# Performance work log

Hardware: AMD Instinct MI355X
Metric: run time of the kernel (lower is better)

## Reference

```python
import jax, jax.numpy as jnp
import numpy as np

N = 50000      # nodes
E = 800000     # edges
DIN = 256
DH = 256
DOUT = 64


def setup_inputs() -> dict:
    key = jax.random.key(0)
    ks = jax.random.split(key, 8)
    x = jax.random.normal(ks[0], (N, DIN), dtype=jnp.float32)
    edge_index = jax.random.randint(ks[1], (2, E), 0, N, dtype=jnp.int64)
    s = 0.05
    W1 = jax.random.normal(ks[2], (DIN, DH), dtype=jnp.float32) * s
    b1 = jnp.zeros((DH,), dtype=jnp.float32)
    W2 = jax.random.normal(ks[3], (DH, DH), dtype=jnp.float32) * s
    b2 = jnp.zeros((DH,), dtype=jnp.float32)
    W3 = jax.random.normal(ks[4], (DH, DOUT), dtype=jnp.float32) * s
    b3 = jnp.zeros((DOUT,), dtype=jnp.float32)
    return {"x": x, "edge_index": edge_index, "W1": W1, "b1": b1,
            "W2": W2, "b2": b2, "W3": W3, "b3": b3}


def gcn_conv(x, src, dst, deg_inv_sqrt, W, b):
    # x: [N, din] -> [N, dout]. PyG GCNConv: h = D^{-1/2}(A+I)D^{-1/2} (x W) + b
    n = x.shape[0]
    h = x @ W                                   # [N, dout]
    norm = deg_inv_sqrt[src] * deg_inv_sqrt[dst]  # [E+N]
    msgs = h[src] * norm[:, None]               # gather + scale, [E+N, dout]
    out = jax.ops.segment_sum(msgs, dst, num_segments=n)  # scatter-add
    return out + b


def _loops(edge_index, n):
    # add self loops, compute symmetric normalization degrees
    sl = jnp.arange(n, dtype=edge_index.dtype)
    src = jnp.concatenate([edge_index[0], sl])
    dst = jnp.concatenate([edge_index[1], sl])
    deg = jax.ops.segment_sum(jnp.ones_like(dst, dtype=jnp.float32), dst, num_segments=n)
    dis = jnp.where(deg > 0, jax.lax.rsqrt(deg), 0.0)
    return src, dst, dis


def reference(x, edge_index, W1, b1, W2, b2, W3, b3):
    src, dst, dis = _loops(edge_index, x.shape[0])
    h = jax.nn.relu(gcn_conv(x, src, dst, dis, W1, b1))   # dropout: eval no-op
    h = jax.nn.relu(gcn_conv(h, src, dst, dis, W2, b2))
    out = gcn_conv(h, src, dst, dis, W3, b3)              # batch=None -> no pooling
    return out
```

## Files before the change

kernel.cpp:

```cpp
#include <hip/hip_runtime.h>
#include <hip/hip_fp8.h>
#include <cstdint>
#include <cstddef>

typedef unsigned short u16;
typedef _Float16 f16x8 __attribute__((ext_vector_type(8)));
typedef float f32x2 __attribute__((ext_vector_type(2)));
typedef float f32x4 __attribute__((ext_vector_type(4)));

#if defined(__has_builtin)
#if __has_builtin(__builtin_amdgcn_cvt_pk_f32_fp8) && __has_builtin(__builtin_amdgcn_cvt_pk_fp8_f32)
#define FP8_BUILTIN 1
#endif
#endif

__device__ __forceinline__ float h2f(u16 u) {
  return (float)__builtin_bit_cast(_Float16, u);
}
__device__ __forceinline__ u16 f2h(float f) {
  return __builtin_bit_cast(u16, (_Float16)f);
}
__device__ __forceinline__ unsigned char ftofp8(float f) {
#ifdef FP8_BUILTIN
  return (unsigned char)(__builtin_amdgcn_cvt_pk_fp8_f32(f, f, 0, false) & 0xFF);
#else
  return __hip_fp8_e4m3(f).__x;
#endif
}

__device__ __forceinline__ void async16(u16* lds, const u16* g) {
  __builtin_amdgcn_global_load_lds(
      (const __attribute__((address_space(1))) unsigned int*)g,
      (__attribute__((address_space(3))) unsigned int*)lds, 16, 0, 0);
}

__device__ __forceinline__ void fma8p(float* a, float d, uint2 p) {
#ifdef FP8_BUILTIN
  f32x2 v0 = __builtin_amdgcn_cvt_pk_f32_fp8((int)p.x, false);
  f32x2 v1 = __builtin_amdgcn_cvt_pk_f32_fp8((int)p.x, true);
  f32x2 v2 = __builtin_amdgcn_cvt_pk_f32_fp8((int)p.y, false);
  f32x2 v3 = __builtin_amdgcn_cvt_pk_f32_fp8((int)p.y, true);
  a[0] += d * v0.x; a[1] += d * v0.y; a[2] += d * v1.x; a[3] += d * v1.y;
  a[4] += d * v2.x; a[5] += d * v2.y; a[6] += d * v3.x; a[7] += d * v3.y;
#else
  const unsigned char* b = (const unsigned char*)&p;
#pragma unroll
  for (int k = 0; k < 8; ++k) {
    __hip_fp8_e4m3 v; v.__x = b[k];
    a[k] += d * (float)v;
  }
#endif
}

__device__ __forceinline__ f16x8 cvt8(const float* p) {
  float4 a = *(const float4*)p;
  float4 b = *(const float4*)(p + 4);
  f16x8 r;
  r[0] = (_Float16)a.x; r[1] = (_Float16)a.y; r[2] = (_Float16)a.z; r[3] = (_Float16)a.w;
  r[4] = (_Float16)b.x; r[5] = (_Float16)b.y; r[6] = (_Float16)b.z; r[7] = (_Float16)b.w;
  return r;
}

__device__ __forceinline__ int wave_is64(const void* ep) {
  const unsigned* p = (const unsigned*)ep;
  const int lane = threadIdx.x & 63;
  unsigned v = p[2 * lane + 1] | p[2 * (lane + 64) + 1];
  unsigned long long bal = __ballot(v != 0u);
  return (bal == 0ull) ? 1 : 0;
}

__device__ __forceinline__ int edge_at(const void* ep, int is64, long long idx) {
  if (is64) return (int)((const long long*)ep)[idx];
  return ((const int*)ep)[idx];
}

#define NCHUNK 64

__global__ void zero_f32(float* p, int n) {
  int i = blockIdx.x * 256 + threadIdx.x;
  if (i < n) p[i] = 0.f;
}

__global__ __launch_bounds__(256) void prep_all(
    const float* __restrict__ W1, u16* __restrict__ wt1,
    const float* __restrict__ W2, u16* __restrict__ wt2,
    const float* __restrict__ W3, u16* __restrict__ wt3,
    const void* __restrict__ ep, int* __restrict__ cnt,
    int E, int N, int DIN, int DH, int DOUT,
    int nb_w1, int nb_w2, int nb_w3) {
  int b = blockIdx.x;
  if (b < nb_w1) {
    int idx = b * 256 + threadIdx.x;
    if (idx < DIN * DH) {
      int n = idx / DIN, k = idx % DIN;
      wt1[idx] = f2h(W1[k * DH + n]);
    }
    return;
  }
  b -= nb_w1;
  if (b < nb_w2) {
    int idx = b * 256 + threadIdx.x;
    if (idx < DH * DH) {
      int n = idx / DH, k = idx % DH;
      wt2[idx] = f2h(W2[k * DH + n]);
    }
    return;
  }
  b -= nb_w2;
  if (b < nb_w3) {
    int idx = b * 256 + threadIdx.x;
    if (idx < DH * DOUT) {
      int n = idx / DH, k = idx % DH;
      wt3[idx] = f2h(W3[k * DOUT + n]);
    }
    return;
  }
  b -= nb_w3;
  {
    __shared__ int h[256];
    h[threadIdx.x] = 0;
    __syncthreads();
    int is64 = wave_is64(ep);
    const int per = (E + NCHUNK - 1) / NCHUNK;
    const int e0 = b * per, e1 = min(e0 + per, E);
    for (int e = e0 + (int)threadIdx.x; e < e1; e += 256) {
      int d = edge_at(ep, is64, (long long)E + e);
      d = min(max(d, 0), N - 1);
      atomicAdd(&h[d >> 8], 1);
    }
    __syncthreads();
    cnt[threadIdx.x * NCHUNK + b] = h[threadIdx.x];
  }
}

__device__ __forceinline__ void bases_in_lds(const int* __restrict__ cnt,
                                             int nbuck, int E, int* bl, int* ws4) {
  const int t = threadIdx.x, lane = t & 63, w = t >> 6;
  int tot = 0;
  if (t < nbuck)
#pragma unroll 8
    for (int c = 0; c < NCHUNK; ++c) tot += cnt[t * NCHUNK + c];
  int inc = tot;
#pragma unroll
  for (int o = 1; o < 64; o <<= 1) {
    int u = __shfl_up(inc, o, 64);
    if (lane >= o) inc += u;
  }
  if (lane == 63) ws4[w] = inc;
  __syncthreads();
  if (t == 0) {
    int run = 0;
#pragma unroll
    for (int k = 0; k < 4; ++k) { int v = ws4[k]; ws4[k + 4] = run; run += v; }
  }
  __syncthreads();
  bl[t] = ws4[w + 4] + inc - tot;
  if (t == 0) bl[nbuck] = E;
  __syncthreads();
}

__global__ __launch_bounds__(256) void csr_bucket(const void* __restrict__ ep,
                                                  const int* __restrict__ cnt,
                                                  unsigned* __restrict__ tmp,
                                                  int E, int N, int nbuck) {
  __shared__ int bl[257];
  __shared__ int cur[256];
  __shared__ int ws4[8];
  const int chunk = blockIdx.x;
  const int t = threadIdx.x;
  bases_in_lds(cnt, nbuck, E, bl, ws4);
  if (t < nbuck) {
    int partial = 0;
    for (int c = 0; c < chunk; ++c) partial += cnt[t * NCHUNK + c];
    cur[t] = bl[t] + partial;
  }
  __syncthreads();
  int is64 = wave_is64(ep);
  const int per = (E + NCHUNK - 1) / NCHUNK;
  const int e0 = chunk * per, e1 = min(e0 + per, E);
  for (int e = e0 + t; e < e1; e += 256) {
    int s = edge_at(ep, is64, e);
    int d = edge_at(ep, is64, (long long)E + e);
    s = min(max(s, 0), N - 1);
    d = min(max(d, 0), N - 1);
    int pos = atomicAdd(&cur[d >> 8], 1);
    tmp[pos] = ((unsigned)d << 16) | (unsigned)s;
  }
}

__global__ __launch_bounds__(256) void csr_final(const unsigned* __restrict__ tmp,
                                                 const int* __restrict__ cnt,
                                                 int* __restrict__ rp,
                                                 float* __restrict__ dis,
                                                 u16* __restrict__ col,
                                                 int N, int E, int nbuck) {
  __shared__ int bl[257];
  __shared__ int hcnt[256];
  __shared__ int curs[256];
  __shared__ int ws4[8];
  const int b = blockIdx.x;
  const int node0 = b * 256;
  const int t = threadIdx.x, lane = t & 63, w = t >> 6;
  bases_in_lds(cnt, nbuck, E, bl, ws4);
  const int k0 = bl[b], k1 = bl[b + 1];
  hcnt[t] = 0;
  __syncthreads();
  for (int k = k0 + t; k < k1; k += 256)
    atomicAdd(&hcnt[(int)(tmp[k] >> 16) - node0], 1);
  __syncthreads();
  const int v = hcnt[t];
  int inc = v;
#pragma unroll
  for (int o = 1; o < 64; o <<= 1) {
    int u = __shfl_up(inc, o, 64);
    if (lane >= o) inc += u;
  }
  __syncthreads();
  if (lane == 63) ws4[w] = inc;
  __syncthreads();
  if (t == 0) {
    int run = 0;
#pragma unroll
    for (int k = 0; k < 4; ++k) { int vv = ws4[k]; ws4[k + 4] = run; run += vv; }
  }
  __syncthreads();
  const int excl = k0 + ws4[w + 4] + inc - v;
  if (node0 + t < N) {
    rp[node0 + t] = excl;
    dis[node0 + t] = rsqrtf((float)(v + 1));
  }
  if (b == 0 && t == 0) rp[N] = E;
  curs[t] = excl;
  __syncthreads();
  for (int k = k0 + t; k < k1; k += 256) {
    unsigned e = tmp[k];
    int dl = (int)(e >> 16) - node0;
    int pos = atomicAdd(&curs[dl], 1);
    col[pos] = (u16)(e & 0xFFFFu);
  }
}

template <int BN, int OUT8, int A32>
__global__ __launch_bounds__(256) void gemm_bres(const void* __restrict__ A,
                                                 const u16* __restrict__ Bt,
                                                 void* __restrict__ Cv, int Nt,
                                                 int Nrows) {
  constexpr int K = 256;
  constexpr int NJ = BN / 16;
  constexpr int CH = BN * K / 8;
  __shared__ __align__(16) u16 Bs[BN * K];

  const int tid = threadIdx.x, lane = tid & 63, w = tid >> 6;
  const int bm = blockIdx.x, bn = blockIdx.y;

#pragma unroll
  for (int i = 0; i < CH / 256; ++i) {
    int c = tid + i * 256;
    int ln = c & 63, t2 = c >> 6;
    int ks = t2 & 7, j = t2 >> 3;
    int row = j * 16 + (ln & 15);
    int kk = ks * 32 + (ln >> 4) * 8;
    async16(&Bs[(size_t)c * 8], Bt + (size_t)(bn * BN + row) * K + kk);
  }

  const int r16 = lane & 15, quad = lane >> 4;
  const int m0 = w * 32;

  int row0 = bm * 128 + m0 + r16;
  int row1 = row0 + 16;
  f16x8 aa0[8], aa1[8];
  if (A32) {
    row0 = min(row0, Nrows - 1);
    row1 = min(row1, Nrows - 1);
    const float* A0 = (const float*)A + (size_t)row0 * K + quad * 8;
    const float* A1 = (const float*)A + (size_t)row1 * K + quad * 8;
#pragma unroll
    for (int ks = 0; ks < 8; ++ks) {
      aa0[ks] = cvt8(A0 + ks * 32);
      aa1[ks] = cvt8(A1 + ks * 32);
    }
  } else {
    const u16* A0 = (const u16*)A + (size_t)row0 * K + quad * 8;
    const u16* A1 = (const u16*)A + (size_t)row1 * K + quad * 8;
#pragma unroll
    for (int ks = 0; ks < 8; ++ks) {
      aa0[ks] = *(const f16x8*)(A0 + ks * 32);
      aa1[ks] = *(const f16x8*)(A1 + ks * 32);
    }
  }

  f32x4 acc[2][NJ];
  const f32x4 fzero = {0.f, 0.f, 0.f, 0.f};
#pragma unroll
  for (int i = 0; i < 2; ++i)
#pragma unroll
    for (int j = 0; j < NJ; ++j) acc[i][j] = fzero;

  __syncthreads();

#pragma unroll
  for (int ks = 0; ks < 8; ++ks) {
#pragma unroll
    for (int j = 0; j < NJ; ++j) {
      f16x8 bf = *(const f16x8*)(&Bs[(size_t)((j * 8 + ks) * 64 + lane) * 8]);
      acc[0][j] = __builtin_amdgcn_mfma_f32_16x16x32_f16(aa0[ks], bf, acc[0][j], 0, 0, 0);
      acc[1][j] = __builtin_amdgcn_mfma_f32_16x16x32_f16(aa1[ks], bf, acc[1][j], 0, 0, 0);
    }
  }
#pragma unroll
  for (int i = 0; i < 2; ++i)
#pragma unroll
    for (int j = 0; j < NJ; ++j) {
      int gr = bm * 128 + m0 + i * 16 + quad * 4;
      int gc = bn * BN + j * 16 + r16;
#pragma unroll
      for (int r = 0; r < 4; ++r) {
        if (OUT8) {
          ((unsigned char*)Cv)[(size_t)(gr + r) * Nt + gc] = ftofp8(acc[i][j][r]);
        } else {
          ((u16*)Cv)[(size_t)(gr + r) * Nt + gc] = f2h(acc[i][j][r]);
        }
      }
    }
}

__global__ __launch_bounds__(256) void agg_d256(const unsigned char* __restrict__ h,
                                                const int* __restrict__ rp,
                                                const u16* __restrict__ col,
                                                const float* __restrict__ dis,
                                                const float* __restrict__ bias,
                                                u16* __restrict__ out, int N) {
  const int wid = threadIdx.x >> 6, lane = threadIdx.x & 63;
  const int i = blockIdx.x * 4 + wid;
  if (i >= N) return;
  const int sub = lane >> 5;
  const int l32 = lane & 31;
  const int c8 = l32 * 8;
  const float di = dis[i];
  float a[8] = {0.f, 0.f, 0.f, 0.f, 0.f, 0.f, 0.f, 0.f};
  if (sub == 0) {
    uint2 sv = *(const uint2*)(h + (size_t)i * 256 + c8);
    fma8p(a, di, sv);
  }
  const int e1 = rp[i + 1];
  for (int base = rp[i]; base < e1; base += 64) {
    int me = base + lane;
    int s_l = 0; float d_l = 0.f;
    if (me < e1) { s_l = (int)col[me]; d_l = dis[s_l]; }
    const int cnt = min(64, e1 - base);
    const int cntR = (cnt + 7) & ~7;
    for (int t = 0; t < cntR; t += 8) {
      int sA = __shfl(s_l, t + sub, 64);      float dA = __shfl(d_l, t + sub, 64);
      int sB = __shfl(s_l, t + 2 + sub, 64);  float dB = __shfl(d_l, t + 2 + sub, 64);
      int sC = __shfl(s_l, t + 4 + sub, 64);  float dC = __shfl(d_l, t + 4 + sub, 64);
      int sD = __shfl(s_l, t + 6 + sub, 64);  float dD = __shfl(d_l, t + 6 + sub, 64);
      uint2 pA = *(const uint2*)(h + (size_t)sA * 256 + c8);
      uint2 pB = *(const uint2*)(h + (size_t)sB * 256 + c8);
      uint2 pC = *(const uint2*)(h + (size_t)sC * 256 + c8);
      uint2 pD = *(const uint2*)(h + (size_t)sD * 256 + c8);
      fma8p(a, dA, pA); fma8p(a, dB, pB); fma8p(a, dC, pC); fma8p(a, dD, pD);
    }
  }
#pragma unroll
  for (int k = 0; k < 8; ++k) a[k] += __shfl_xor(a[k], 32, 64);
  if (sub == 0) {
    float4 b0 = *(const float4*)(bias + c8);
    float4 b1 = *(const float4*)(bias + c8 + 4);
    float r0 = fmaxf(di * a[0] + b0.x, 0.f), r1 = fmaxf(di * a[1] + b0.y, 0.f);
    float r2 = fmaxf(di * a[2] + b0.z, 0.f), r3 = fmaxf(di * a[3] + b0.w, 0.f);
    float r4 = fmaxf(di * a[4] + b1.x, 0.f), r5 = fmaxf(di * a[5] + b1.y, 0.f);
    float r6 = fmaxf(di * a[6] + b1.z, 0.f), r7 = fmaxf(di * a[7] + b1.w, 0.f);
    uint4 ov;
    ov.x = (unsigned)f2h(r0) | ((unsigned)f2h(r1) << 16);
    ov.y = (unsigned)f2h(r2) | ((unsigned)f2h(r3) << 16);
    ov.z = (unsigned)f2h(r4) | ((unsigned)f2h(r5) << 16);
    ov.w = (unsigned)f2h(r6) | ((unsigned)f2h(r7) << 16);
    *(uint4*)(out + (size_t)i * 256 + c8) = ov;
  }
}

__global__ __launch_bounds__(256) void agg_d64(const unsigned char* __restrict__ h,
                                               const int* __restrict__ rp,
                                               const u16* __restrict__ col,
                                               const float* __restrict__ dis,
                                               const float* __restrict__ bias,
                                               float* __restrict__ out, int N) {
  const int wid = threadIdx.x >> 6, lane = threadIdx.x & 63;
  const int i = blockIdx.x * 4 + wid;
  if (i >= N) return;
  const int grp = lane >> 3;
  const int l8 = lane & 7;
  const int c8 = l8 * 8;
  const float di = dis[i];
  float a[8] = {0.f, 0.f, 0.f, 0.f, 0.f, 0.f, 0.f, 0.f};
  if (grp == 0) {
    uint2 sv = *(const uint2*)(h + (size_t)i * 64 + c8);
    fma8p(a, di, sv);
  }
  const int e1 = rp[i + 1];
  for (int base = rp[i]; base < e1; base += 64) {
    int me = base + lane;
    int s_l = 0; float d_l = 0.f;
    if (me < e1) { s_l = (int)col[me]; d_l = dis[s_l]; }
    const int cnt = min(64, e1 - base);
    const int cntR = (cnt + 15) & ~15;
    for (int t = 0; t < cntR; t += 16) {
      int sA = __shfl(s_l, t + grp, 64);       float dA = __shfl(d_l, t + grp, 64);
      int sB = __shfl(s_l, t + 8 + grp, 64);   float dB = __shfl(d_l, t + 8 + grp, 64);
      uint2 pA = *(const uint2*)(h + (size_t)sA * 64 + c8);
      uint2 pB = *(const uint2*)(h + (size_t)sB * 64 + c8);
      fma8p(a, dA, pA); fma8p(a, dB, pB);
    }
  }
#pragma unroll
  for (int k = 0; k < 8; ++k) a[k] += __shfl_xor(a[k], 8, 64);
#pragma unroll
  for (int k = 0; k < 8; ++k) a[k] += __shfl_xor(a[k], 16, 64);
#pragma unroll
  for (int k = 0; k < 8; ++k) a[k] += __shfl_xor(a[k], 32, 64);
  if (lane < 8) {
    float4 b0 = *(const float4*)(bias + c8);
    float4 b1 = *(const float4*)(bias + c8 + 4);
    float4 o0, o1;
    o0.x = di * a[0] + b0.x; o0.y = di * a[1] + b0.y;
    o0.z = di * a[2] + b0.z; o0.w = di * a[3] + b0.w;
    o1.x = di * a[4] + b1.x; o1.y = di * a[5] + b1.y;
    o1.z = di * a[6] + b1.z; o1.w = di * a[7] + b1.w;
    *(float4*)(out + (size_t)i * 64 + c8) = o0;
    *(float4*)(out + (size_t)i * 64 + c8 + 4) = o1;
  }
}

extern "C" void kernel_launch(void* const* d_in, const int* in_sizes, int n_in,
                              void* d_out, int out_size, void* d_ws, size_t ws_size,
                              hipStream_t stream) {
  if (n_in < 8) return;
  const float* x = (const float*)d_in[0];
  const void* eptr = d_in[1];
  const float* W1 = (const float*)d_in[2];
  const float* b1 = (const float*)d_in[3];
  const float* W2 = (const float*)d_in[4];
  const float* b2 = (const float*)d_in[5];
  const float* W3 = (const float*)d_in[6];
  const float* b3 = (const float*)d_in[7];
  float* out = (float*)d_out;

  const int DIN = 256, DH = 256;
  const int N = in_sizes[0] / DIN;
  const int E = in_sizes[1] / 2;
  const int DOUT = in_sizes[6] / DH;
  const int MT = (N + 127) / 128;
  const int Mpad = MT * 128;
  const int nbuck = (N + 255) >> 8;

  auto rnd = [](size_t b) { return (b + 255) & ~(size_t)255; };
  size_t required = 0;
  required += rnd((size_t)Mpad * DH * 2);
  required += rnd((size_t)Mpad * DH);
  required += rnd((size_t)E * 2);
  required += rnd((size_t)E * 4);
  required += rnd((size_t)(N + 1) * 4);
  required += rnd((size_t)N * 4);
  required += rnd((size_t)DIN * DH * 2);
  required += rnd((size_t)DH * DH * 2);
  required += rnd((size_t)DH * DOUT * 2);
  required += rnd((size_t)256 * NCHUNK * 4);
  if (ws_size < required || N > 65536 || nbuck > 256 || nbuck < 1) {
    zero_f32<<<(out_size + 255) / 256, 256, 0, stream>>>(out, out_size);
    return;
  }

  char* ws = (char*)d_ws;
  size_t off0 = 0;
  auto alloc = [&](size_t bytes) {
    char* p = ws + off0;
    off0 = (off0 + bytes + 255) & ~(size_t)255;
    return p;
  };
  u16* xpad = (u16*)alloc((size_t)Mpad * DH * 2);
  unsigned char* hbuf = (unsigned char*)alloc((size_t)Mpad * DH);
  u16* colb = (u16*)alloc((size_t)E * 2);
  unsigned* tmpb = (unsigned*)alloc((size_t)E * 4);
  int* rp = (int*)alloc((size_t)(N + 1) * 4);
  float* dis = (float*)alloc((size_t)N * 4);
  u16* wt1 = (u16*)alloc((size_t)DIN * DH * 2);
  u16* wt2 = (u16*)alloc((size_t)DH * DH * 2);
  u16* wt3 = (u16*)alloc((size_t)DH * DOUT * 2);
  int* cnt = (int*)alloc((size_t)256 * NCHUNK * 4);

  const int nb_w1 = (DIN * DH + 255) / 256;
  const int nb_w2 = (DH * DH + 255) / 256;
  const int nb_w3 = (DH * DOUT + 255) / 256;
  prep_all<<<nb_w1 + nb_w2 + nb_w3 + NCHUNK, 256, 0, stream>>>(
      W1, wt1, W2, wt2, W3, wt3, eptr, cnt,
      E, N, DIN, DH, DOUT, nb_w1, nb_w2, nb_w3);

  csr_bucket<<<NCHUNK, 256, 0, stream>>>(eptr, cnt, tmpb, E, N, nbuck);
  csr_final<<<nbuck, 256, 0, stream>>>(tmpb, cnt, rp, dis, colb, N, E, nbuck);

  gemm_bres<128, 1, 1><<<dim3(MT, DH / 128), 256, 0, stream>>>(x, wt1, hbuf, DH, N);
  agg_d256<<<(N + 3) / 4, 256, 0, stream>>>(hbuf, rp, colb, dis, b1, xpad, N);
  gemm_bres<128, 1, 0><<<dim3(MT, DH / 128), 256, 0, stream>>>(xpad, wt2, hbuf, DH, N);
  agg_d256<<<(N + 3) / 4, 256, 0, stream>>>(hbuf, rp, colb, dis, b2, xpad, N);
  gemm_bres<64, 1, 0><<<dim3(MT, DOUT / 64), 256, 0, stream>>>(xpad, wt3, hbuf, DOUT, N);
  agg_d64<<<(N + 3) / 4, 256, 0, stream>>>(hbuf, rp, colb, dis, b3, out, N);
}
```

Baseline: 297.1 us.

## Fold source-degree scaling into aggregation outputs and use fp16 final layer

The aggregation kernels now multiply their output rows by the source normalization dis[i] before writing. The following GEMM therefore produces pre-scaled features, and the next aggregation no longer has to load and shuffle per-edge dis values. The second layer carries a ×4 fp8 scale that is undone at the end. The last GEMM writes fp16 instead of fp8, which doubles the gather bytes for the 64-wide layer. CSR chunking also grows from 64 to 256 with a transposed count layout for coalesced reads, and a guard is added for small E or DOUT != 64.

```diff
diff --git a/kernel.cpp b/kernel.cpp
--- a/kernel.cpp
+++ b/kernel.cpp
@@ -19,6 +19,9 @@
 }
 __device__ __forceinline__ u16 f2h(float f) {
   return __builtin_bit_cast(u16, (_Float16)f);
+}
+__device__ __forceinline__ unsigned pkh(float lo, float hi) {
+  return (unsigned)f2h(lo) | ((unsigned)f2h(hi) << 16);
 }
 __device__ __forceinline__ unsigned char ftofp8(float f) {
 #ifdef FP8_BUILTIN
@@ -34,22 +37,28 @@
       (__attribute__((address_space(3))) unsigned int*)lds, 16, 0, 0);
 }
 
-__device__ __forceinline__ void fma8p(float* a, float d, uint2 p) {
+__device__ __forceinline__ void fma8p2(f32x2* a2, float d, uint2 p) {
 #ifdef FP8_BUILTIN
+  f32x2 d2; d2[0] = d; d2[1] = d;
   f32x2 v0 = __builtin_amdgcn_cvt_pk_f32_fp8((int)p.x, false);
   f32x2 v1 = __builtin_amdgcn_cvt_pk_f32_fp8((int)p.x, true);
   f32x2 v2 = __builtin_amdgcn_cvt_pk_f32_fp8((int)p.y, false);
   f32x2 v3 = __builtin_amdgcn_cvt_pk_f32_fp8((int)p.y, true);
-  a[0] += d * v0.x; a[1] += d * v0.y; a[2] += d * v1.x; a[3] += d * v1.y;
-  a[4] += d * v2.x; a[5] += d * v2.y; a[6] += d * v3.x; a[7] += d * v3.y;
+  a2[0] += d2 * v0; a2[1] += d2 * v1; a2[2] += d2 * v2; a2[3] += d2 * v3;
 #else
   const unsigned char* b = (const unsigned char*)&p;
 #pragma unroll
   for (int k = 0; k < 8; ++k) {
     __hip_fp8_e4m3 v; v.__x = b[k];
-    a[k] += d * (float)v;
+    a2[k >> 1][k & 1] += d * (float)v;
   }
 #endif
+}
+
+__device__ __forceinline__ void fma8h(float* a, float d, uint4 p) {
+  const u16* q = (const u16*)&p;
+#pragma unroll
+  for (int k = 0; k < 8; ++k) a[k] += d * h2f(q[k]);
 }
 
 __device__ __forceinline__ f16x8 cvt8(const float* p) {
@@ -74,7 +83,7 @@
   return ((const int*)ep)[idx];
 }
 
-#define NCHUNK 64
+#define NCHUNK 256
 
 __global__ void zero_f32(float* p, int n) {
   int i = blockIdx.x * 256 + threadIdx.x;
@@ -129,7 +138,7 @@
       atomicAdd(&h[d >> 8], 1);
     }
     __syncthreads();
-    cnt[threadIdx.x * NCHUNK + b] = h[threadIdx.x];
+    cnt[b * 256 + threadIdx.x] = h[threadIdx.x];
   }
 }
 
@@ -137,9 +146,10 @@
                                              int nbuck, int E, int* bl, int* ws4) {
   const int t = threadIdx.x, lane = t & 63, w = t >> 6;
   int tot = 0;
-  if (t < nbuck)
-#pragma unroll 8
-    for (int c = 0; c < NCHUNK; ++c) tot += cnt[t * NCHUNK + c];
+  if (t < nbuck) {
+#pragma unroll 4
+    for (int c = 0; c < NCHUNK; ++c) tot += cnt[c * 256 + t];
+  }
   int inc = tot;
 #pragma unroll
   for (int o = 1; o < 64; o <<= 1) {
@@ -171,7 +181,7 @@
   bases_in_lds(cnt, nbuck, E, bl, ws4);
   if (t < nbuck) {
     int partial = 0;
-    for (int c = 0; c < chunk; ++c) partial += cnt[t * NCHUNK + c];
+    for (int c = 0; c < chunk; ++c) partial += cnt[c * 256 + t];
     cur[t] = bl[t] + partial;
   }
   __syncthreads();
@@ -240,7 +250,7 @@
   }
 }
 
-template <int BN, int OUT8, int A32>
+template <int BN, int OUT8, int A32, int SC>
 __global__ __launch_bounds__(256) void gemm_bres(const void* __restrict__ A,
                                                  const u16* __restrict__ Bt,
                                                  void* __restrict__ Cv, int Nt,
@@ -316,7 +326,8 @@
 #pragma unroll
       for (int r = 0; r < 4; ++r) {
         if (OUT8) {
-          ((unsigned char*)Cv)[(size_t)(gr + r) * Nt + gc] = ftofp8(acc[i][j][r]);
+          ((unsigned char*)Cv)[(size_t)(gr + r) * Nt + gc] =
+              ftofp8(acc[i][j][r] * (float)SC);
         } else {
           ((u16*)Cv)[(size_t)(gr + r) * Nt + gc] = f2h(acc[i][j][r]);
         }
@@ -324,6 +335,7 @@
     }
 }
 
+template <int SCALED>
 __global__ __launch_bounds__(256) void agg_d256(const unsigned char* __restrict__ h,
                                                 const int* __restrict__ rp,
                                                 const u16* __restrict__ col,
@@ -337,49 +349,67 @@
   const int l32 = lane & 31;
   const int c8 = l32 * 8;
   const float di = dis[i];
-  float a[8] = {0.f, 0.f, 0.f, 0.f, 0.f, 0.f, 0.f, 0.f};
+  f32x2 a2[4];
+#pragma unroll
+  for (int k = 0; k < 4; ++k) { a2[k][0] = 0.f; a2[k][1] = 0.f; }
   if (sub == 0) {
     uint2 sv = *(const uint2*)(h + (size_t)i * 256 + c8);
-    fma8p(a, di, sv);
+    fma8p2(a2, SCALED ? 1.f : di, sv);
   }
   const int e1 = rp[i + 1];
   for (int base = rp[i]; base < e1; base += 64) {
     int me = base + lane;
     int s_l = 0; float d_l = 0.f;
-    if (me < e1) { s_l = (int)col[me]; d_l = dis[s_l]; }
+    if (me < e1) { s_l = (int)col[me]; if (!SCALED) d_l = dis[s_l]; }
     const int cnt = min(64, e1 - base);
     const int cntR = (cnt + 7) & ~7;
     for (int t = 0; t < cntR; t += 8) {
-      int sA = __shfl(s_l, t + sub, 64);      float dA = __shfl(d_l, t + sub, 64);
-      int sB = __shfl(s_l, t + 2 + sub, 64);  float dB = __shfl(d_l, t + 2 + sub, 64);
-      int sC = __shfl(s_l, t + 4 + sub, 64);  float dC = __shfl(d_l, t + 4 + sub, 64);
-      int sD = __shfl(s_l, t + 6 + sub, 64);  float dD = __shfl(d_l, t + 6 + sub, 64);
+      int sA = __shfl(s_l, t + sub, 64);
+      int sB = __shfl(s_l, t + 2 + sub, 64);
+      int sC = __shfl(s_l, t + 4 + sub, 64);
+      int sD = __shfl(s_l, t + 6 + sub, 64);
+      float dA, dB, dC, dD;
+      if (SCALED) {
+        dA = (t + sub < cnt) ? 1.f : 0.f;
+        dB = (t + 2 + sub < cnt) ? 1.f : 0.f;
+        dC = (t + 4 + sub < cnt) ? 1.f : 0.f;
+        dD = (t + 6 + sub < cnt) ? 1.f : 0.f;
+      } else {
+        dA = __shfl(d_l, t + sub, 64);
+        dB = __shfl(d_l, t + 2 + sub, 64);
+        dC = __shfl(d_l, t + 4 + sub, 64);
+        dD = __shfl(d_l, t + 6 + sub, 64);
+      }
       uint2 pA = *(const uint2*)(h + (size_t)sA * 256 + c8);
       uint2 pB = *(const uint2*)(h + (size_t)sB * 256 + c8);
       uint2 pC = *(const uint2*)(h + (size_t)sC * 256 + c8);
       uint2 pD = *(const uint2*)(h + (size_t)sD * 256 + c8);
-      fma8p(a, dA, pA); fma8p(a, dB, pB); fma8p(a, dC, pC); fma8p(a, dD, pD);
-    }
-  }
-#pragma unroll
-  for (int k = 0; k < 8; ++k) a[k] += __shfl_xor(a[k], 32, 64);
+      fma8p2(a2, dA, pA); fma8p2(a2, dB, pB);
+      fma8p2(a2, dC, pC); fma8p2(a2, dD, pD);
+    }
+  }
+#pragma unroll
+  for (int k = 0; k < 4; ++k) {
+    a2[k][0] += __shfl_xor(a2[k][0], 32, 64);
+    a2[k][1] += __shfl_xor(a2[k][1], 32, 64);
+  }
   if (sub == 0) {
+    const float inv = SCALED ? 0.25f : 1.f;
     float4 b0 = *(const float4*)(bias + c8);
     float4 b1 = *(const float4*)(bias + c8 + 4);
-    float r0 = fmaxf(di * a[0] + b0.x, 0.f), r1 = fmaxf(di * a[1] + b0.y, 0.f);
-    float r2 = fmaxf(di * a[2] + b0.z, 0.f), r3 = fmaxf(di * a[3] + b0.w, 0.f);
-    float r4 = fmaxf(di * a[4] + b1.x, 0.f), r5 = fmaxf(di * a[5] + b1.y, 0.f);
-    float r6 = fmaxf(di * a[6] + b1.z, 0.f), r7 = fmaxf(di * a[7] + b1.w, 0.f);
+    float bb[8] = {b0.x, b0.y, b0.z, b0.w, b1.x, b1.y, b1.z, b1.w};
+    float r[8];
+#pragma unroll
+    for (int k = 0; k < 8; ++k)
+      r[k] = fmaxf(di * a2[k >> 1][k & 1] * inv + bb[k], 0.f) * di;
     uint4 ov;
-    ov.x = (unsigned)f2h(r0) | ((unsigned)f2h(r1) << 16);
-    ov.y = (unsigned)f2h(r2) | ((unsigned)f2h(r3) << 16);
-    ov.z = (unsigned)f2h(r4) | ((unsigned)f2h(r5) << 16);
-    ov.w = (unsigned)f2h(r6) | ((unsigned)f2h(r7) << 16);
+    ov.x = pkh(r[0], r[1]); ov.y = pkh(r[2], r[3]);
+    ov.z = pkh(r[4], r[5]); ov.w = pkh(r[6], r[7]);
     *(uint4*)(out + (size_t)i * 256 + c8) = ov;
   }
 }
 
-__global__ __launch_bounds__(256) void agg_d64(const unsigned char* __restrict__ h,
+__global__ __launch_bounds__(256) void agg_d64(const u16* __restrict__ h,
                                                const int* __restrict__ rp,
                                                const u16* __restrict__ col,
                                                const float* __restrict__ dis,
@@ -394,22 +424,24 @@
   const float di = dis[i];
   float a[8] = {0.f, 0.f, 0.f, 0.f, 0.f, 0.f, 0.f, 0.f};
   if (grp == 0) {
-    uint2 sv = *(const uint2*)(h + (size_t)i * 64 + c8);
-    fma8p(a, di, sv);
+    uint4 sv = *(const uint4*)(h + (size_t)i * 64 + c8);
+    fma8h(a, 1.f, sv);
   }
   const int e1 = rp[i + 1];
   for (int base = rp[i]; base < e1; base += 64) {
     int me = base + lane;
-    int s_l = 0; float d_l = 0.f;
-    if (me < e1) { s_l = (int)col[me]; d_l = dis[s_l]; }
+    int s_l = 0;
+    if (me < e1) s_l = (int)col[me];
     const int cnt = min(64, e1 - base);
     const int cntR = (cnt + 15) & ~15;
     for (int t = 0; t < cntR; t += 16) {
-      int sA = __shfl(s_l, t + grp, 64);       float dA = __shfl(d_l, t + grp, 64);
-      int sB = __shfl(s_l, t + 8 + grp, 64);   float dB = __shfl(d_l, t + 8 + grp, 64);
-      uint2 pA = *(const uint2*)(h + (size_t)sA * 64 + c8);
-      uint2 pB = *(const uint2*)(h + (size_t)sB * 64 + c8);
-      fma8p(a, dA, pA); fma8p(a, dB, pB);
+      int sA = __shfl(s_l, t + grp, 64);
+      int sB = __shfl(s_l, t + 8 + grp, 64);
+      float dA = (t + grp < cnt) ? 1.f : 0.f;
+      float dB = (t + 8 + grp < cnt) ? 1.f : 0.f;
+      uint4 pA = *(const uint4*)(h + (size_t)sA * 64 + c8);
+      uint4 pB = *(const uint4*)(h + (size_t)sB * 64 + c8);
+      fma8h(a, dA, pA); fma8h(a, dB, pB);
     }
   }
 #pragma unroll
@@ -465,7 +497,8 @@
   required += rnd((size_t)DH * DH * 2);
   required += rnd((size_t)DH * DOUT * 2);
   required += rnd((size_t)256 * NCHUNK * 4);
-  if (ws_size < required || N > 65536 || nbuck > 256 || nbuck < 1) {
+  if (ws_size < required || N > 65536 || nbuck > 256 || nbuck < 1 ||
+      E < 128 || DOUT != 64) {
     zero_f32<<<(out_size + 255) / 256, 256, 0, stream>>>(out, out_size);
     return;
   }
@@ -498,10 +531,14 @@
   csr_bucket<<<NCHUNK, 256, 0, stream>>>(eptr, cnt, tmpb, E, N, nbuck);
   csr_final<<<nbuck, 256, 0, stream>>>(tmpb, cnt, rp, dis, colb, N, E, nbuck);
 
-  gemm_bres<128, 1, 1><<<dim3(MT, DH / 128), 256, 0, stream>>>(x, wt1, hbuf, DH, N);
-  agg_d256<<<(N + 3) / 4, 256, 0, stream>>>(hbuf, rp, colb, dis, b1, xpad, N);
-  gemm_bres<128, 1, 0><<<dim3(MT, DH / 128), 256, 0, stream>>>(xpad, wt2, hbuf, DH, N);
-  agg_d256<<<(N + 3) / 4, 256, 0, stream>>>(hbuf, rp, colb, dis, b2, xpad, N);
-  gemm_bres<64, 1, 0><<<dim3(MT, DOUT / 64), 256, 0, stream>>>(xpad, wt3, hbuf, DOUT, N);
-  agg_d64<<<(N + 3) / 4, 256, 0, stream>>>(hbuf, rp, colb, dis, b3, out, N);
-}
+  gemm_bres<128, 1, 1, 1><<<dim3(MT, DH / 128), 256, 0, stream>>>(
+      x, wt1, hbuf, DH, N);
+  agg_d256<0><<<(N + 3) / 4, 256, 0, stream>>>(hbuf, rp, colb, dis, b1, xpad, N);
+  gemm_bres<128, 1, 0, 4><<<dim3(MT, DH / 128), 256, 0, stream>>>(
+      xpad, wt2, hbuf, DH, N);
+  agg_d256<1><<<(N + 3) / 4, 256, 0, stream>>>(hbuf, rp, colb, dis, b2, xpad, N);
+  gemm_bres<64, 0, 0, 1><<<dim3(MT, DOUT / 64), 256, 0, stream>>>(
+      xpad, wt3, hbuf, DOUT, N);
+  agg_d64<<<(N + 3) / 4, 256, 0, stream>>>((const u16*)hbuf, rp, colb, dis, b3,
+                                           out, N);
+}
```

Measured after the change: 299.7 us. About the same (+0.9%).
